# Optimization experiments

Measured on AMD Instinct MI355X. Metric: run time of the kernel, lower is better.

The kernel has to match this reference:

```python
import jax, jax.numpy as jnp
import numpy as np

# Sizes: batch, mapper input dim, subspace dim n, ambient dim k (= n, no equalities),
# number of linear inequalities, number of quadratic constraints.
B, IN_DIM, N, K, M_LIN, QC = 32768, 256, 128, 128, 1024, 16


def setup_inputs() -> dict:
    rng = np.random.default_rng(0)
    x = rng.standard_normal((B, IN_DIM, 1), dtype=np.float32)
    # mapper = nn.Linear(IN_DIM, N)
    W = (rng.standard_normal((N, IN_DIM)) / np.sqrt(IN_DIM)).astype(np.float32)
    b = (0.01 * rng.standard_normal((N,))).astype(np.float32)
    # Linear inequalities A_p z <= b_p, strictly feasible at z0 = 0
    z0 = np.zeros((N, 1), dtype=np.float32)
    A_p = rng.standard_normal((M_LIN, N)).astype(np.float32)
    b_p = (A_p @ z0 + rng.uniform(0.5, 1.5, (M_LIN, 1))).astype(np.float32)
    D = (A_p / (b_p - A_p @ z0)).astype(np.float32)  # D = A_p / ((b_p - A_p z0) 1^T)
    # No equality constraints: y = NA_E z + yp with NA_E = I, yp = 0, y0 = z0
    NA_E = np.eye(K, N, dtype=np.float32)
    yp = np.zeros((K, 1), dtype=np.float32)
    y0 = NA_E @ z0 + yp
    # Quadratic constraints 0.5 y'P y + q'y + r <= 0, strictly feasible at y0.
    # Precompute phi, delta exactly as in ConstraintModule.__init__ (RAYEN branch).
    all_phi = np.empty((QC, 1, K), dtype=np.float32)
    all_delta = np.empty((QC, K, K), dtype=np.float32)
    for i in range(QC):
        G = (rng.standard_normal((K, K)) / np.sqrt(K)).astype(np.float32)
        P = G.T @ G + 0.1 * np.eye(K, dtype=np.float32)
        q = (0.1 * rng.standard_normal((K, 1))).astype(np.float32)
        val0 = 0.5 * y0.T @ P @ y0 + q.T @ y0
        r = -(val0 + np.float32(rng.uniform(0.5, 2.0)))  # value at y0 strictly negative
        quad_at_y0 = 0.5 * y0.T @ P @ y0 + q.T @ y0 + r   # [1,1], < 0
        sigma = 2.0 * quad_at_y0                           # scalar < 0
        g = y0.T @ P + q.T                                 # [1,K]
        all_phi[i] = -g / sigma
        all_delta[i] = (g.T @ g - 4.0 * quad_at_y0 * 0.5 * P) / np.square(sigma)
    return {
        "x": jnp.asarray(x),
        "W": jnp.asarray(W),
        "b": jnp.asarray(b),
        "D": jnp.asarray(D),
        "NA_E": jnp.asarray(NA_E),
        "yp": jnp.asarray(yp),
        "z0": jnp.asarray(z0),
        "all_phi": jnp.asarray(all_phi),
        "all_delta": jnp.asarray(all_delta),
    }


def reference(x, W, b, D, NA_E, yp, z0, all_phi, all_delta):
    Bn = x.shape[0]
    # mapper: x.view(B,-1) -> Linear -> unsqueeze(2)
    v = (x.reshape(Bn, -1) @ W.T + b)[:, :, None]                     # [B,n,1]
    norm_v = jnp.sqrt(jnp.sum(v * v, axis=(1, 2), keepdims=True))    # [B,1,1]
    v_bar = v / jnp.maximum(norm_v, 1e-12)                           # F.normalize
    # kappa from linear constraints: relu(max_m (D v_bar)_m)
    Dv = jnp.einsum('mn,bno->bmo', D, v_bar)                         # [B,M,1]
    kappa = jax.nn.relu(jnp.max(Dv, axis=1, keepdims=True))          # [B,1,1]
    # kappa from quadratic constraints: phi_i rho + sqrt(rho' delta_i rho)
    rho = jnp.einsum('kn,bno->bko', NA_E, v_bar)[..., 0]             # [B,k]
    lin_term = rho @ all_phi[:, 0, :].T                              # [B,Q]
    dr = jnp.einsum('qkl,bl->bqk', all_delta, rho)                   # [B,Q,k]
    quad_term = jnp.einsum('bqk,bk->bq', dr, rho)                    # [B,Q]
    kappa_q = lin_term + jnp.sqrt(quad_term)                         # [B,Q]
    kappa_nl = jnp.max(kappa_q, axis=1)[:, None, None]               # [B,1,1]
    kappa = jnp.maximum(kappa, kappa_nl)
    # alpha = min(1/kappa, ||v||); z = z0 + alpha * v_bar; y = NA_E z + yp
    alpha = jnp.minimum(1.0 / kappa, norm_v)
    z = z0 + alpha * v_bar                                           # [B,n,1]
    y = jnp.einsum('kn,bno->bko', NA_E, z) + yp                      # [B,k,1]
    return y
```

## Files before the change

### kernel.cpp

```cpp
#include <hip/hip_runtime.h>
#include <hip/hip_bf16.h>


typedef __attribute__((ext_vector_type(8))) short short8;
typedef __attribute__((ext_vector_type(4))) float f32x4;

__device__ __forceinline__ float bf2f(unsigned short u) {
    union { unsigned int i; float f; } v; v.i = ((unsigned int)u) << 16; return v.f;
}
__device__ __forceinline__ unsigned short f2bf(float f) {
    union { float f; unsigned int i; } v; v.f = f;
    unsigned int r = v.i + 0x7FFFu + ((v.i >> 16) & 1u);
    return (unsigned short)(r >> 16);
}

template<int DT>
__device__ __forceinline__ short8 ld8(const void* p, size_t i) {
    if constexpr (DT == 1) {
        return *reinterpret_cast<const short8*>(reinterpret_cast<const unsigned short*>(p) + i);
    } else {
        const float* f = reinterpret_cast<const float*>(p) + i;
        short8 r;
#pragma unroll
        for (int j = 0; j < 8; ++j) r[j] = (short)f2bf(f[j]);
        return r;
    }
}
template<int DT>
__device__ __forceinline__ float ldf(const void* p, int i) {
    if constexpr (DT == 1) return bf2f(reinterpret_cast<const unsigned short*>(p)[i]);
    else return reinterpret_cast<const float*>(p)[i];
}

__device__ __forceinline__ void glds16(const void* g, void* l) {
    __builtin_amdgcn_global_load_lds(
        (const __attribute__((address_space(1))) void*)g,
        (__attribute__((address_space(3))) void*)l, 16, 0, 0);
}

__global__ void detect_dtype(const unsigned short* __restrict__ x, int* __restrict__ flag) {
    __shared__ int cnt;
    if (threadIdx.x == 0) cnt = 0;
    __syncthreads();
    float a = fabsf(bf2f(x[threadIdx.x]));
    int ok = (a > 1e-3f && a < 1e2f) ? 1 : 0;
    atomicAdd(&cnt, ok);
    __syncthreads();
    if (threadIdx.x == 0) *flag = (cnt > 200) ? 1 : 0;
}

template<int DT>
__global__ __launch_bounds__(256, 2) void k1_vbar(
    const void* __restrict__ xp, const void* __restrict__ Wp, const void* __restrict__ bp,
    unsigned short* __restrict__ rho_g, unsigned int* __restrict__ kap_u,
    const int* __restrict__ flag)
{
    if (*flag != DT) return;
    __shared__ unsigned char lds_x[32768];
    __shared__ unsigned char lds_v[16384];
    __shared__ float lds_nsq[64][4];

    const int tid = threadIdx.x;
    const int lane = tid & 63;
    const int w = tid >> 6, hi = lane >> 4, lo = lane & 15;
    const size_t row0 = (size_t)blockIdx.x * 64;
    const unsigned char* Xb = (const unsigned char*)xp;

#pragma unroll
    for (int i = 0; i < 8; ++i) {
        int ch = i * 256 + tid;
        int row = ((ch >> 9) << 4) | (ch & 15);
        int off = (((ch >> 6) & 7) << 6) | (((ch >> 4) & 3) << 4);
        if constexpr (DT == 1)
            glds16(Xb + (row0 + row) * 512 + off, lds_x + ch * 16);
        else {
            short8 v = ld8<0>(Xb, (row0 + row) * 256 + (off >> 1));
            *reinterpret_cast<short8*>(lds_x + ch * 16) = v;
        }
    }
    short8 wf[2][8];
#pragma unroll
    for (int ct = 0; ct < 2; ++ct)
#pragma unroll
        for (int kb = 0; kb < 8; ++kb)
            wf[ct][kb] = ld8<DT>(Wp, (size_t)(w * 32 + ct * 16 + lo) * 256 + kb * 32 + hi * 8);
    asm volatile("s_waitcnt vmcnt(0)" ::: "memory");
    __syncthreads();

    f32x4 acc1[2][4];
#pragma unroll
    for (int c = 0; c < 2; ++c)
#pragma unroll
        for (int r = 0; r < 4; ++r)
#pragma unroll
            for (int e = 0; e < 4; ++e) acc1[c][r][e] = 0.f;
#pragma unroll
    for (int kb = 0; kb < 8; ++kb) {
        short8 af[4];
#pragma unroll
        for (int rt = 0; rt < 4; ++rt)
            af[rt] = *reinterpret_cast<const short8*>(lds_x + (((rt << 3) | kb) << 10) + lane * 16);
#pragma unroll
        for (int ct = 0; ct < 2; ++ct)
#pragma unroll
            for (int rt = 0; rt < 4; ++rt)
                acc1[ct][rt] = __builtin_amdgcn_mfma_f32_16x16x32_bf16(af[rt], wf[ct][kb], acc1[ct][rt], 0, 0, 0);
    }
    float bv[2];
#pragma unroll
    for (int ct = 0; ct < 2; ++ct) bv[ct] = ldf<DT>(bp, w * 32 + ct * 16 + lo);
#pragma unroll
    for (int rt = 0; rt < 4; ++rt)
#pragma unroll
        for (int reg = 0; reg < 4; ++reg) {
            float s = 0.f;
#pragma unroll
            for (int ct = 0; ct < 2; ++ct) {
                float v = acc1[ct][rt][reg] + bv[ct];
                acc1[ct][rt][reg] = v;
                s += v * v;
            }
            s += __shfl_xor(s, 1); s += __shfl_xor(s, 2);
            s += __shfl_xor(s, 4); s += __shfl_xor(s, 8);
            if (lo == 0) lds_nsq[rt * 16 + hi * 4 + reg][w] = s;
        }
    __syncthreads();

#pragma unroll
    for (int rt = 0; rt < 4; ++rt)
#pragma unroll
        for (int reg = 0; reg < 4; ++reg) {
            int row = rt * 16 + hi * 4 + reg;
            float nsq = lds_nsq[row][0] + lds_nsq[row][1] + lds_nsq[row][2] + lds_nsq[row][3];
            float rinv = 1.0f / fmaxf(sqrtf(nsq), 1e-12f);
#pragma unroll
            for (int ct = 0; ct < 2; ++ct) {
                int col = w * 32 + ct * 16 + lo;
                *reinterpret_cast<unsigned short*>(lds_v + row * 256 + col * 2) =
                    f2bf(acc1[ct][rt][reg] * rinv);
            }
        }
    if (tid < 64) {
        float nsq = lds_nsq[tid][0] + lds_nsq[tid][1] + lds_nsq[tid][2] + lds_nsq[tid][3];
        float norm = sqrtf(nsq);
        kap_u[row0 + tid] = __float_as_uint(1.0f / norm);
    }
    __syncthreads();
#pragma unroll
    for (int i = 0; i < 4; ++i) {
        int ch = i * 256 + tid;
        int row = ch >> 4, c16 = ch & 15;
        *reinterpret_cast<short8*>(rho_g + (row0 + row) * 128 + c16 * 8) =
            *reinterpret_cast<const short8*>(lds_v + row * 256 + c16 * 16);
    }
}

__device__ __forceinline__ void stage_rho(const unsigned short* rho_g, size_t row0,
                                          unsigned char* lds_rho, int tid) {
#pragma unroll
    for (int i = 0; i < 4; ++i) {
        int ch = i * 256 + tid;
        int row = ch >> 4;
        int off = (ch & 15) * 16;
        glds16((const unsigned char*)rho_g + (row0 + row) * 256 + (off ^ ((row & 7) << 4)),
               lds_rho + ch * 16);
    }
}

template<int DT>
__global__ __launch_bounds__(256, 2) void k2a_dmax(
    const void* __restrict__ Dp, const unsigned short* __restrict__ rho_g,
    unsigned int* __restrict__ kap_u, const int* __restrict__ flag)
{
    if (*flag != DT) return;
    __shared__ unsigned char lds_rho[16384];
    __shared__ float lds_red[64][4];
    const int tid = threadIdx.x;
    const int lane = tid & 63;
    const int w = tid >> 6, hi = lane >> 4, lo = lane & 15;
    const size_t row0 = (size_t)blockIdx.x * 64;
    const int mg = blockIdx.y;

    stage_rho(rho_g, row0, lds_rho, tid);
    asm volatile("s_waitcnt vmcnt(0)" ::: "memory");
    __syncthreads();

    short8 af2[4][4];
#pragma unroll
    for (int rt = 0; rt < 4; ++rt)
#pragma unroll
        for (int kb = 0; kb < 4; ++kb) {
            int row = rt * 16 + lo;
            af2[rt][kb] = *reinterpret_cast<const short8*>(
                lds_rho + row * 256 + (((kb << 6) | (hi << 4)) ^ ((lo & 7) << 4)));
        }

    f32x4 dmax[4];
#pragma unroll
    for (int rt = 0; rt < 4; ++rt)
#pragma unroll
        for (int e = 0; e < 4; ++e) dmax[rt][e] = -3e38f;

#pragma unroll 2
    for (int t = 0; t < 4; ++t) {
        int col = mg * 256 + w * 64 + t * 16 + lo;
        short8 bD[4];
#pragma unroll
        for (int kb = 0; kb < 4; ++kb)
            bD[kb] = ld8<DT>(Dp, (size_t)col * 128 + kb * 32 + hi * 8);
        f32x4 acc[4];
#pragma unroll
        for (int rt = 0; rt < 4; ++rt)
#pragma unroll
            for (int e = 0; e < 4; ++e) acc[rt][e] = 0.f;
#pragma unroll
        for (int kb = 0; kb < 4; ++kb)
#pragma unroll
            for (int rt = 0; rt < 4; ++rt)
                acc[rt] = __builtin_amdgcn_mfma_f32_16x16x32_bf16(af2[rt][kb], bD[kb], acc[rt], 0, 0, 0);
#pragma unroll
        for (int rt = 0; rt < 4; ++rt)
#pragma unroll
            for (int e = 0; e < 4; ++e) dmax[rt][e] = fmaxf(dmax[rt][e], acc[rt][e]);
    }
#pragma unroll
    for (int rt = 0; rt < 4; ++rt)
#pragma unroll
        for (int reg = 0; reg < 4; ++reg) {
            float m = dmax[rt][reg];
            m = fmaxf(m, __shfl_xor(m, 1)); m = fmaxf(m, __shfl_xor(m, 2));
            m = fmaxf(m, __shfl_xor(m, 4)); m = fmaxf(m, __shfl_xor(m, 8));
            if (lo == 0) lds_red[rt * 16 + hi * 4 + reg][w] = m;
        }
    __syncthreads();
    if (tid < 64) {
        float m = fmaxf(fmaxf(lds_red[tid][0], lds_red[tid][1]),
                        fmaxf(lds_red[tid][2], lds_red[tid][3]));
        m = fmaxf(m, 0.f);
        atomicMax(&kap_u[row0 + tid], __float_as_uint(m));
    }
}

template<int DT>
__global__ __launch_bounds__(256, 2) void k2b_quad(
    const void* __restrict__ dltp, const void* __restrict__ phip,
    const unsigned short* __restrict__ rho_g,
    unsigned int* __restrict__ kap_u, const int* __restrict__ flag)
{
    if (*flag != DT) return;
    __shared__ unsigned char lds_rho[16384];
    const int tid = threadIdx.x;
    const int lane = tid & 63;
    const int w = tid >> 6, hi = lane >> 4, lo = lane & 15;
    const size_t row0 = (size_t)blockIdx.x * 64;
    const int q = blockIdx.y * 4 + w;

    stage_rho(rho_g, row0, lds_rho, tid);
    asm volatile("s_waitcnt vmcnt(0)" ::: "memory");
    __syncthreads();

    short8 af2[4][4];
#pragma unroll
    for (int rt = 0; rt < 4; ++rt)
#pragma unroll
        for (int kb = 0; kb < 4; ++kb) {
            int row = rt * 16 + lo;
            af2[rt][kb] = *reinterpret_cast<const short8*>(
                lds_rho + row * 256 + (((kb << 6) | (hi << 4)) ^ ((lo & 7) << 4)));
        }

    f32x4 qsum[4], lsum[4];
#pragma unroll
    for (int rt = 0; rt < 4; ++rt)
#pragma unroll
        for (int e = 0; e < 4; ++e) { qsum[rt][e] = 0.f; lsum[rt][e] = 0.f; }

#pragma unroll 2
    for (int t = 0; t < 8; ++t) {
        int colk = t * 16 + lo;
        short8 bq[4];
#pragma unroll
        for (int kb = 0; kb < 4; ++kb)
            bq[kb] = ld8<DT>(dltp, ((size_t)q * 128 + colk) * 128 + kb * 32 + hi * 8);
        float phv = ldf<DT>(phip, q * 128 + colk);
        f32x4 acc[4];
#pragma unroll
        for (int rt = 0; rt < 4; ++rt)
#pragma unroll
            for (int e = 0; e < 4; ++e) acc[rt][e] = 0.f;
#pragma unroll
        for (int kb = 0; kb < 4; ++kb)
#pragma unroll
            for (int rt = 0; rt < 4; ++rt)
                acc[rt] = __builtin_amdgcn_mfma_f32_16x16x32_bf16(af2[rt][kb], bq[kb], acc[rt], 0, 0, 0);
#pragma unroll
        for (int rt = 0; rt < 4; ++rt)
#pragma unroll
            for (int e = 0; e < 4; ++e) {
                int row = rt * 16 + hi * 4 + e;
                float rv = bf2f(*reinterpret_cast<const unsigned short*>(
                    lds_rho + row * 256 + ((colk * 2) ^ ((row & 7) << 4))));
                qsum[rt][e] += acc[rt][e] * rv;
                lsum[rt][e] += rv * phv;
            }
    }
#pragma unroll
    for (int rt = 0; rt < 4; ++rt)
#pragma unroll
        for (int reg = 0; reg < 4; ++reg) {
            float s = qsum[rt][reg];
            s += __shfl_xor(s, 1); s += __shfl_xor(s, 2);
            s += __shfl_xor(s, 4); s += __shfl_xor(s, 8);
            float l = lsum[rt][reg];
            l += __shfl_xor(l, 1); l += __shfl_xor(l, 2);
            l += __shfl_xor(l, 4); l += __shfl_xor(l, 8);
            if (lo == 0) {
                float kq = l + sqrtf(fmaxf(s, 0.f));
                kq = fmaxf(kq, 0.f);
                atomicMax(&kap_u[row0 + rt * 16 + hi * 4 + reg], __float_as_uint(kq));
            }
        }
}

template<int DT>
__global__ __launch_bounds__(256, 2) void k3_out(
    const unsigned int* __restrict__ kap_u,
    const void* __restrict__ z0p, const void* __restrict__ ypp,
    unsigned short* __restrict__ outp, const int* __restrict__ flag)
{
    if (*flag != DT) return;
    __shared__ float lds_alpha[64];
    const int tid = threadIdx.x;
    const size_t row0 = (size_t)blockIdx.x * 64;

    if (tid < 64)
        lds_alpha[tid] = 1.0f / __uint_as_float(kap_u[row0 + tid]);
    __syncthreads();
#pragma unroll
    for (int i = 0; i < 4; ++i) {
        int idx = tid + i * 256;
        int row = idx >> 4;
        int col0 = (idx & 15) * 8;
        float alpha = lds_alpha[row];
        size_t obase = (row0 + row) * 128 + col0;
        short8 r8 = *reinterpret_cast<const short8*>(outp + obase);
        short8 pack;
#pragma unroll
        for (int j = 0; j < 8; ++j) {
            float yv = ldf<DT>(z0p, col0 + j) + alpha * bf2f((unsigned short)r8[j])
                     + ldf<DT>(ypp, col0 + j);
            pack[j] = (short)f2bf(yv);
        }
        *reinterpret_cast<short8*>(outp + obase) = pack;
    }
}

template<int DT>
__global__ __launch_bounds__(256, 2) void rayen_mono(
    const void* xp, const void* Wp, const void* bp, const void* Dp,
    const void* ypp, const void* z0p, const void* phip, const void* dltp,
    void* outp, const int* flag)
{
    if (*flag != DT) return;
    __shared__ unsigned char lds_big[49152];
    __shared__ unsigned char lds_rho[16384];
    __shared__ float lds_nsq[64][4];
    __shared__ float lds_dmax[64][4];
    __shared__ float lds_quad[64][16];
    __shared__ float lds_lin[64][16];
    __shared__ float lds_alpha[64];

    const int tid = threadIdx.x;
    const int lane = tid & 63;
    const int w = tid >> 6, hi = lane >> 4, lo = lane & 15;
    const size_t row0 = (size_t)blockIdx.x * 64;
    const unsigned char* Xb = (const unsigned char*)xp;

#pragma unroll
    for (int i = 0; i < 8; ++i) {
        int ch = i * 256 + tid;
        int row = ((ch >> 9) << 4) | (ch & 15);
        int off = (((ch >> 6) & 7) << 6) | (((ch >> 4) & 3) << 4);
        if constexpr (DT == 1)
            glds16(Xb + (row0 + row) * 512 + off, lds_big + ch * 16);
        else {
            short8 v = ld8<0>(Xb, (row0 + row) * 256 + (off >> 1));
            *reinterpret_cast<short8*>(lds_big + ch * 16) = v;
        }
    }
    short8 wf[2][8];
#pragma unroll
    for (int ct = 0; ct < 2; ++ct)
#pragma unroll
        for (int kb = 0; kb < 8; ++kb)
            wf[ct][kb] = ld8<DT>(Wp, (size_t)(w * 32 + ct * 16 + lo) * 256 + kb * 32 + hi * 8);
    asm volatile("s_waitcnt vmcnt(0)" ::: "memory");
    __syncthreads();

    f32x4 acc1[2][4];
#pragma unroll
    for (int c = 0; c < 2; ++c)
#pragma unroll
        for (int r = 0; r < 4; ++r)
#pragma unroll
            for (int e = 0; e < 4; ++e) acc1[c][r][e] = 0.f;
#pragma unroll
    for (int kb = 0; kb < 8; ++kb) {
        short8 af[4];
#pragma unroll
        for (int rt = 0; rt < 4; ++rt)
            af[rt] = *reinterpret_cast<const short8*>(lds_big + (((rt << 3) | kb) << 10) + lane * 16);
#pragma unroll
        for (int ct = 0; ct < 2; ++ct)
#pragma unroll
            for (int rt = 0; rt < 4; ++rt)
                acc1[ct][rt] = __builtin_amdgcn_mfma_f32_16x16x32_bf16(af[rt], wf[ct][kb], acc1[ct][rt], 0, 0, 0);
    }
    float bv[2];
#pragma unroll
    for (int ct = 0; ct < 2; ++ct) bv[ct] = ldf<DT>(bp, w * 32 + ct * 16 + lo);
#pragma unroll
    for (int rt = 0; rt < 4; ++rt)
#pragma unroll
        for (int reg = 0; reg < 4; ++reg) {
            float s = 0.f;
#pragma unroll
            for (int ct = 0; ct < 2; ++ct) {
                float v = acc1[ct][rt][reg] + bv[ct];
                acc1[ct][rt][reg] = v;
                s += v * v;
            }
            s += __shfl_xor(s, 1); s += __shfl_xor(s, 2);
            s += __shfl_xor(s, 4); s += __shfl_xor(s, 8);
            if (lo == 0) lds_nsq[rt * 16 + hi * 4 + reg][w] = s;
        }
    __syncthreads();
#pragma unroll
    for (int rt = 0; rt < 4; ++rt)
#pragma unroll
        for (int reg = 0; reg < 4; ++reg) {
            int row = rt * 16 + hi * 4 + reg;
            float nsq = lds_nsq[row][0] + lds_nsq[row][1] + lds_nsq[row][2] + lds_nsq[row][3];
            float rinv = 1.0f / fmaxf(sqrtf(nsq), 1e-12f);
#pragma unroll
            for (int ct = 0; ct < 2; ++ct) {
                int col = w * 32 + ct * 16 + lo;
                *reinterpret_cast<unsigned short*>(
                    lds_rho + row * 256 + ((col * 2) ^ ((row & 7) << 4))) =
                    f2bf(acc1[ct][rt][reg] * rinv);
            }
        }
    __syncthreads();
    short8 af2[4][4];
#pragma unroll
    for (int rt = 0; rt < 4; ++rt)
#pragma unroll
        for (int kb = 0; kb < 4; ++kb) {
            int row = rt * 16 + lo;
            af2[rt][kb] = *reinterpret_cast<const short8*>(
                lds_rho + row * 256 + (((kb << 6) | (hi << 4)) ^ ((lo & 7) << 4)));
        }
    unsigned char* wbase = lds_big + w * 12288;
    auto stage_q = [&](int p, int b) {
        unsigned char* dst0 = wbase + b * 4096;
#pragma unroll
        for (int kb = 0; kb < 4; ++kb) {
            size_t grow; const void* base;
            if (p < 16) { base = Dp; grow = (size_t)(p * 64 + w * 16 + lo); }
            else {
                int pd = p - 16;
                base = dltp;
                grow = (size_t)((((pd >> 3) * 4 + w) * 128) + ((pd & 7) * 16 + lo));
            }
            if constexpr (DT == 1)
                glds16((const unsigned char*)base + grow * 256 + kb * 64 + hi * 16, dst0 + kb * 1024);
            else {
                short8 v = ld8<0>(base, grow * 128 + kb * 32 + hi * 8);
                *reinterpret_cast<short8*>(dst0 + kb * 1024 + lane * 16) = v;
            }
        }
    };
    f32x4 dmax[4], qsum[4];
#pragma unroll
    for (int rt = 0; rt < 4; ++rt)
#pragma unroll
        for (int e = 0; e < 4; ++e) { dmax[rt][e] = -3e38f; qsum[rt][e] = 0.f; }
    stage_q(0, 0); stage_q(1, 1);
#pragma unroll 1
    for (int p = 0; p < 48; ++p) {
        if constexpr (DT == 1) {
            if (p < 47) { asm volatile("s_waitcnt vmcnt(4)" ::: "memory"); }
            else        { asm volatile("s_waitcnt vmcnt(0)" ::: "memory"); }
        } else {
            asm volatile("s_waitcnt vmcnt(0) lgkmcnt(0)" ::: "memory");
        }
        __builtin_amdgcn_sched_barrier(0);
        if (p + 2 < 48) stage_q(p + 2, (p + 2) % 3);
        unsigned char* buf = wbase + (p % 3) * 4096;
        f32x4 acc[4];
#pragma unroll
        for (int rt = 0; rt < 4; ++rt)
#pragma unroll
            for (int e = 0; e < 4; ++e) acc[rt][e] = 0.f;
#pragma unroll
        for (int kb = 0; kb < 4; ++kb) {
            short8 bf = *reinterpret_cast<const short8*>(buf + kb * 1024 + lane * 16);
#pragma unroll
            for (int rt = 0; rt < 4; ++rt)
                acc[rt] = __builtin_amdgcn_mfma_f32_16x16x32_bf16(af2[rt][kb], bf, acc[rt], 0, 0, 0);
        }
        if (p < 16) {
#pragma unroll
            for (int rt = 0; rt < 4; ++rt)
#pragma unroll
                for (int e = 0; e < 4; ++e) dmax[rt][e] = fmaxf(dmax[rt][e], acc[rt][e]);
        } else {
            int pd = p - 16, kr = (pd & 7) << 4;
#pragma unroll
            for (int rt = 0; rt < 4; ++rt)
#pragma unroll
                for (int e = 0; e < 4; ++e) {
                    int row = rt * 16 + hi * 4 + e;
                    float rvv = bf2f(*reinterpret_cast<const unsigned short*>(
                        lds_rho + row * 256 + ((((kr + lo) * 2)) ^ ((row & 7) << 4))));
                    qsum[rt][e] += acc[rt][e] * rvv;
                }
            if ((pd & 7) == 7) {
#pragma unroll
                for (int rt = 0; rt < 4; ++rt)
#pragma unroll
                    for (int e = 0; e < 4; ++e) {
                        float s = qsum[rt][e];
                        s += __shfl_xor(s, 1); s += __shfl_xor(s, 2);
                        s += __shfl_xor(s, 4); s += __shfl_xor(s, 8);
                        if (lo == 0) lds_quad[rt * 16 + hi * 4 + e][((pd >> 3) << 2) | w] = s;
                        qsum[rt][e] = 0.f;
                    }
            }
        }
    }
#pragma unroll
    for (int rt = 0; rt < 4; ++rt)
#pragma unroll
        for (int reg = 0; reg < 4; ++reg) {
            float m = dmax[rt][reg];
            m = fmaxf(m, __shfl_xor(m, 1)); m = fmaxf(m, __shfl_xor(m, 2));
            m = fmaxf(m, __shfl_xor(m, 4)); m = fmaxf(m, __shfl_xor(m, 8));
            if (lo == 0) lds_dmax[rt * 16 + hi * 4 + reg][w] = m;
        }
    if (w == 0) {
        f32x4 accp[4];
#pragma unroll
        for (int rt = 0; rt < 4; ++rt)
#pragma unroll
            for (int e = 0; e < 4; ++e) accp[rt][e] = 0.f;
#pragma unroll
        for (int kb = 0; kb < 4; ++kb) {
            short8 bp8 = ld8<DT>(phip, (size_t)lo * 128 + kb * 32 + hi * 8);
#pragma unroll
            for (int rt = 0; rt < 4; ++rt)
                accp[rt] = __builtin_amdgcn_mfma_f32_16x16x32_bf16(af2[rt][kb], bp8, accp[rt], 0, 0, 0);
        }
#pragma unroll
        for (int rt = 0; rt < 4; ++rt)
#pragma unroll
            for (int reg = 0; reg < 4; ++reg)
                lds_lin[rt * 16 + hi * 4 + reg][lo] = accp[rt][reg];
    }
    __syncthreads();
    if (tid < 64) {
        int row = tid;
        float nsq = lds_nsq[row][0] + lds_nsq[row][1] + lds_nsq[row][2] + lds_nsq[row][3];
        float norm = sqrtf(nsq);
        float kap = fmaxf(0.f, fmaxf(fmaxf(lds_dmax[row][0], lds_dmax[row][1]),
                                     fmaxf(lds_dmax[row][2], lds_dmax[row][3])));
#pragma unroll
        for (int q = 0; q < 16; ++q)
            kap = fmaxf(kap, lds_lin[row][q] + sqrtf(fmaxf(lds_quad[row][q], 0.f)));
        lds_alpha[row] = fminf(1.0f / kap, norm);
    }
    __syncthreads();
#pragma unroll
    for (int i = 0; i < 4; ++i) {
        int idx = tid + i * 256;
        int row = idx >> 4, col0 = (idx & 15) * 8;
        float alpha = lds_alpha[row];
        short8 r8 = *reinterpret_cast<const short8*>(
            lds_rho + row * 256 + ((col0 * 2) ^ ((row & 7) << 4)));
        float yv[8];
#pragma unroll
        for (int j = 0; j < 8; ++j)
            yv[j] = ldf<DT>(z0p, col0 + j) + alpha * bf2f((unsigned short)r8[j]) + ldf<DT>(ypp, col0 + j);
        size_t obase = (row0 + row) * 128 + col0;
        if constexpr (DT == 1) {
            short8 pack;
#pragma unroll
            for (int j = 0; j < 8; ++j) pack[j] = (short)f2bf(yv[j]);
            *reinterpret_cast<short8*>(reinterpret_cast<unsigned short*>(outp) + obase) = pack;
        } else {
            f32x4 p0, p1;
#pragma unroll
            for (int j = 0; j < 4; ++j) { p0[j] = yv[j]; p1[j] = yv[4 + j]; }
            *reinterpret_cast<f32x4*>(reinterpret_cast<float*>(outp) + obase) = p0;
            *reinterpret_cast<f32x4*>(reinterpret_cast<float*>(outp) + obase + 4) = p1;
        }
    }
}

extern "C" void kernel_launch(void* const* d_in, const int* in_sizes, int n_in,
                              void* d_out, int out_size, void* d_ws, size_t ws_size,
                              hipStream_t stream) {
    const void* x    = d_in[0];
    const void* W    = d_in[1];
    const void* b    = d_in[2];
    const void* D    = d_in[3];
    const void* yp   = d_in[5];
    const void* z0   = d_in[6];
    const void* phi  = d_in[7];
    const void* dlt  = d_in[8];

    const int B = in_sizes[0] / 256;
    const int tiles = B / 64;

    unsigned char* ws = reinterpret_cast<unsigned char*>(d_ws);
    int* flag = reinterpret_cast<int*>(ws);
    unsigned int* kap_u = reinterpret_cast<unsigned int*>(ws + 4096);
    const size_t need = 4096 + (size_t)B * 4;

    detect_dtype<<<dim3(1), dim3(256), 0, stream>>>(
        reinterpret_cast<const unsigned short*>(x), flag);

    dim3 blk(256);
    if (ws_size >= need) {
        unsigned short* rho_g = reinterpret_cast<unsigned short*>(d_out);
        k1_vbar<1><<<dim3(tiles), blk, 0, stream>>>(x, W, b, rho_g, kap_u, flag);
        k2a_dmax<1><<<dim3(tiles, 4), blk, 0, stream>>>(D, rho_g, kap_u, flag);
        k2b_quad<1><<<dim3(tiles, 4), blk, 0, stream>>>(dlt, phi, rho_g, kap_u, flag);
        k3_out<1><<<dim3(tiles), blk, 0, stream>>>(kap_u, z0, yp, rho_g, flag);
        rayen_mono<0><<<dim3(tiles), blk, 0, stream>>>(x, W, b, D, yp, z0, phi, dlt, d_out, flag);
    } else {
        rayen_mono<1><<<dim3(tiles), blk, 0, stream>>>(x, W, b, D, yp, z0, phi, dlt, d_out, flag);
        rayen_mono<0><<<dim3(tiles), blk, 0, stream>>>(x, W, b, D, yp, z0, phi, dlt, d_out, flag);
    }
}
```

Measured before the change: 127.7 us.

## Route fp32 inputs through split kernels using pre-converted bf16 constants

Adds a cvt_const kernel that converts W, D, delta and phi to bf16 in workspace on every call. The fp32 path then runs the multi-kernel pipeline (vbar, dmax, quad, out) instead of the monolithic rayen_mono kernel. rho is now kept in workspace rather than in the output buffer, and k3_out gains an fp32 store path. fp32 loads of x are vectorised into float4 reads. This is meant to remove the repeated per-block fp32→bf16 conversion of constants and to reuse the split schedule for fp32. In exchange it adds a conversion launch, two extra launches that exit early on the dtype flag, and a much larger workspace requirement; if the workspace is too small, execution falls back to the monolithic kernel.

After: 113.7 us. 1.12x faster.

```diff
diff --git a/kernel.cpp b/kernel.cpp
--- a/kernel.cpp
+++ b/kernel.cpp
@@ -4,6 +4,7 @@
 
 typedef __attribute__((ext_vector_type(8))) short short8;
 typedef __attribute__((ext_vector_type(4))) float f32x4;
+typedef __attribute__((ext_vector_type(4))) unsigned short us4;
 
 __device__ __forceinline__ float bf2f(unsigned short u) {
     union { unsigned int i; float f; } v; v.i = ((unsigned int)u) << 16; return v.f;
@@ -32,6 +33,15 @@
     else return reinterpret_cast<const float*>(p)[i];
 }
 
+__device__ __forceinline__ short8 ld8f4(const float* f) {
+    f32x4 a = *reinterpret_cast<const f32x4*>(f);
+    f32x4 b = *reinterpret_cast<const f32x4*>(f + 4);
+    short8 r;
+#pragma unroll
+    for (int j = 0; j < 4; ++j) { r[j] = (short)f2bf(a[j]); r[4 + j] = (short)f2bf(b[j]); }
+    return r;
+}
+
 __device__ __forceinline__ void glds16(const void* g, void* l) {
     __builtin_amdgcn_global_load_lds(
         (const __attribute__((address_space(1))) void*)g,
@@ -49,9 +59,37 @@
     if (threadIdx.x == 0) *flag = (cnt > 200) ? 1 : 0;
 }
 
+__global__ void cvt_const(
+    const void* __restrict__ Wp, const void* __restrict__ Dp,
+    const void* __restrict__ Qp, const void* __restrict__ Pp,
+    unsigned short* __restrict__ Wb, unsigned short* __restrict__ Db,
+    unsigned short* __restrict__ Qb, unsigned short* __restrict__ Pb,
+    const int* __restrict__ flag)
+{
+    const int nW = 32768, nD = 131072, nQ = 262144, nP = 2048;
+    int idx = blockIdx.x * 256 + threadIdx.x;
+    int e = idx * 4;
+    if (e >= nW + nD + nQ + nP) return;
+    const void* src; unsigned short* dst; int off;
+    if      (e < nW)           { src = Wp; dst = Wb; off = e; }
+    else if (e < nW + nD)      { src = Dp; dst = Db; off = e - nW; }
+    else if (e < nW + nD + nQ) { src = Qp; dst = Qb; off = e - nW - nD; }
+    else                       { src = Pp; dst = Pb; off = e - nW - nD - nQ; }
+    us4 out;
+    if (*flag == 0) {
+        f32x4 v = *reinterpret_cast<const f32x4*>(reinterpret_cast<const float*>(src) + off);
+#pragma unroll
+        for (int j = 0; j < 4; ++j) out[j] = f2bf(v[j]);
+    } else {
+        out = *reinterpret_cast<const us4*>(reinterpret_cast<const unsigned short*>(src) + off);
+    }
+    *reinterpret_cast<us4*>(dst + off) = out;
+}
+
 template<int DT>
 __global__ __launch_bounds__(256, 2) void k1_vbar(
-    const void* __restrict__ xp, const void* __restrict__ Wp, const void* __restrict__ bp,
+    const void* __restrict__ xp, const unsigned short* __restrict__ Wb,
+    const void* __restrict__ bp,
     unsigned short* __restrict__ rho_g, unsigned int* __restrict__ kap_u,
     const int* __restrict__ flag)
 {
@@ -64,18 +102,17 @@
     const int lane = tid & 63;
     const int w = tid >> 6, hi = lane >> 4, lo = lane & 15;
     const size_t row0 = (size_t)blockIdx.x * 64;
-    const unsigned char* Xb = (const unsigned char*)xp;
 
 #pragma unroll
     for (int i = 0; i < 8; ++i) {
         int ch = i * 256 + tid;
         int row = ((ch >> 9) << 4) | (ch & 15);
         int off = (((ch >> 6) & 7) << 6) | (((ch >> 4) & 3) << 4);
-        if constexpr (DT == 1)
-            glds16(Xb + (row0 + row) * 512 + off, lds_x + ch * 16);
-        else {
-            short8 v = ld8<0>(Xb, (row0 + row) * 256 + (off >> 1));
-            *reinterpret_cast<short8*>(lds_x + ch * 16) = v;
+        if constexpr (DT == 1) {
+            glds16((const unsigned char*)xp + (row0 + row) * 512 + off, lds_x + ch * 16);
+        } else {
+            const float* src = (const float*)xp + (row0 + row) * 256 + (off >> 1);
+            *reinterpret_cast<short8*>(lds_x + ch * 16) = ld8f4(src);
         }
     }
     short8 wf[2][8];
@@ -83,8 +120,9 @@
     for (int ct = 0; ct < 2; ++ct)
 #pragma unroll
         for (int kb = 0; kb < 8; ++kb)
-            wf[ct][kb] = ld8<DT>(Wp, (size_t)(w * 32 + ct * 16 + lo) * 256 + kb * 32 + hi * 8);
-    asm volatile("s_waitcnt vmcnt(0)" ::: "memory");
+            wf[ct][kb] = *reinterpret_cast<const short8*>(
+                Wb + (size_t)(w * 32 + ct * 16 + lo) * 256 + kb * 32 + hi * 8);
+    if constexpr (DT == 1) { asm volatile("s_waitcnt vmcnt(0)" ::: "memory"); }
     __syncthreads();
 
     f32x4 acc1[2][4];
@@ -142,8 +180,7 @@
         }
     if (tid < 64) {
         float nsq = lds_nsq[tid][0] + lds_nsq[tid][1] + lds_nsq[tid][2] + lds_nsq[tid][3];
-        float norm = sqrtf(nsq);
-        kap_u[row0 + tid] = __float_as_uint(1.0f / norm);
+        kap_u[row0 + tid] = __float_as_uint(1.0f / sqrtf(nsq));
     }
     __syncthreads();
 #pragma unroll
@@ -167,12 +204,10 @@
     }
 }
 
-template<int DT>
 __global__ __launch_bounds__(256, 2) void k2a_dmax(
-    const void* __restrict__ Dp, const unsigned short* __restrict__ rho_g,
-    unsigned int* __restrict__ kap_u, const int* __restrict__ flag)
+    const unsigned short* __restrict__ Db, const unsigned short* __restrict__ rho_g,
+    unsigned int* __restrict__ kap_u)
 {
-    if (*flag != DT) return;
     __shared__ unsigned char lds_rho[16384];
     __shared__ float lds_red[64][4];
     const int tid = threadIdx.x;
@@ -207,7 +242,7 @@
         short8 bD[4];
 #pragma unroll
         for (int kb = 0; kb < 4; ++kb)
-            bD[kb] = ld8<DT>(Dp, (size_t)col * 128 + kb * 32 + hi * 8);
+            bD[kb] = *reinterpret_cast<const short8*>(Db + (size_t)col * 128 + kb * 32 + hi * 8);
         f32x4 acc[4];
 #pragma unroll
         for (int rt = 0; rt < 4; ++rt)
@@ -241,13 +276,10 @@
     }
 }
 
-template<int DT>
 __global__ __launch_bounds__(256, 2) void k2b_quad(
-    const void* __restrict__ dltp, const void* __restrict__ phip,
-    const unsigned short* __restrict__ rho_g,
-    unsigned int* __restrict__ kap_u, const int* __restrict__ flag)
+    const unsigned short* __restrict__ Qb, const unsigned short* __restrict__ Pb,
+    const unsigned short* __restrict__ rho_g, unsigned int* __restrict__ kap_u)
 {
-    if (*flag != DT) return;
     __shared__ unsigned char lds_rho[16384];
     const int tid = threadIdx.x;
     const int lane = tid & 63;
@@ -281,8 +313,9 @@
         short8 bq[4];
 #pragma unroll
         for (int kb = 0; kb < 4; ++kb)
-            bq[kb] = ld8<DT>(dltp, ((size_t)q * 128 + colk) * 128 + kb * 32 + hi * 8);
-        float phv = ldf<DT>(phip, q * 128 + colk);
+            bq[kb] = *reinterpret_cast<const short8*>(
+                Qb + ((size_t)q * 128 + colk) * 128 + kb * 32 + hi * 8);
+        float phv = bf2f(Pb[q * 128 + colk]);
         f32x4 acc[4];
 #pragma unroll
         for (int rt = 0; rt < 4; ++rt)
@@ -315,8 +348,7 @@
             l += __shfl_xor(l, 1); l += __shfl_xor(l, 2);
             l += __shfl_xor(l, 4); l += __shfl_xor(l, 8);
             if (lo == 0) {
-                float kq = l + sqrtf(fmaxf(s, 0.f));
-                kq = fmaxf(kq, 0.f);
+                float kq = fmaxf(l + sqrtf(fmaxf(s, 0.f)), 0.f);
                 atomicMax(&kap_u[row0 + rt * 16 + hi * 4 + reg], __float_as_uint(kq));
             }
         }
@@ -324,9 +356,9 @@
 
 template<int DT>
 __global__ __launch_bounds__(256, 2) void k3_out(
-    const unsigned int* __restrict__ kap_u,
+    const unsigned int* __restrict__ kap_u, const unsigned short* __restrict__ rho_g,
     const void* __restrict__ z0p, const void* __restrict__ ypp,
-    unsigned short* __restrict__ outp, const int* __restrict__ flag)
+    void* __restrict__ outp, const int* __restrict__ flag)
 {
     if (*flag != DT) return;
     __shared__ float lds_alpha[64];
@@ -342,16 +374,29 @@
         int row = idx >> 4;
         int col0 = (idx & 15) * 8;
         float alpha = lds_alpha[row];
+        short8 r8 = *reinterpret_cast<const short8*>(rho_g + (row0 + row) * 128 + col0);
         size_t obase = (row0 + row) * 128 + col0;
-        short8 r8 = *reinterpret_cast<const short8*>(outp + obase);
-        short8 pack;
-#pragma unroll
-        for (int j = 0; j < 8; ++j) {
-            float yv = ldf<DT>(z0p, col0 + j) + alpha * bf2f((unsigned short)r8[j])
-                     + ldf<DT>(ypp, col0 + j);
-            pack[j] = (short)f2bf(yv);
-        }
-        *reinterpret_cast<short8*>(outp + obase) = pack;
+        if constexpr (DT == 1) {
+            short8 pack;
+#pragma unroll
+            for (int j = 0; j < 8; ++j) {
+                float yv = ldf<1>(z0p, col0 + j) + alpha * bf2f((unsigned short)r8[j])
+                         + ldf<1>(ypp, col0 + j);
+                pack[j] = (short)f2bf(yv);
+            }
+            *reinterpret_cast<short8*>(reinterpret_cast<unsigned short*>(outp) + obase) = pack;
+        } else {
+            f32x4 p0, p1;
+#pragma unroll
+            for (int j = 0; j < 4; ++j) {
+                p0[j] = ldf<0>(z0p, col0 + j) + alpha * bf2f((unsigned short)r8[j])
+                      + ldf<0>(ypp, col0 + j);
+                p1[j] = ldf<0>(z0p, col0 + 4 + j) + alpha * bf2f((unsigned short)r8[4 + j])
+                      + ldf<0>(ypp, col0 + 4 + j);
+            }
+            *reinterpret_cast<f32x4*>(reinterpret_cast<float*>(outp) + obase) = p0;
+            *reinterpret_cast<f32x4*>(reinterpret_cast<float*>(outp) + obase + 4) = p1;
+        }
     }
 }
 
@@ -384,8 +429,8 @@
         if constexpr (DT == 1)
             glds16(Xb + (row0 + row) * 512 + off, lds_big + ch * 16);
         else {
-            short8 v = ld8<0>(Xb, (row0 + row) * 256 + (off >> 1));
-            *reinterpret_cast<short8*>(lds_big + ch * 16) = v;
+            const float* src = (const float*)xp + (row0 + row) * 256 + (off >> 1);
+            *reinterpret_cast<short8*>(lds_big + ch * 16) = ld8f4(src);
         }
     }
     short8 wf[2][8];
@@ -475,8 +520,8 @@
             if constexpr (DT == 1)
                 glds16((const unsigned char*)base + grow * 256 + kb * 64 + hi * 16, dst0 + kb * 1024);
             else {
-                short8 v = ld8<0>(base, grow * 128 + kb * 32 + hi * 8);
-                *reinterpret_cast<short8*>(dst0 + kb * 1024 + lane * 16) = v;
+                const float* src = (const float*)base + grow * 128 + kb * 32 + hi * 8;
+                *reinterpret_cast<short8*>(dst0 + kb * 1024 + lane * 16) = ld8f4(src);
             }
         }
     };
@@ -624,20 +669,27 @@
 
     unsigned char* ws = reinterpret_cast<unsigned char*>(d_ws);
     int* flag = reinterpret_cast<int*>(ws);
-    unsigned int* kap_u = reinterpret_cast<unsigned int*>(ws + 4096);
-    const size_t need = 4096 + (size_t)B * 4;
+    unsigned int*   kap_u = reinterpret_cast<unsigned int*>(ws + 4096);
+    unsigned short* Wb    = reinterpret_cast<unsigned short*>(ws + 135168);
+    unsigned short* Db    = reinterpret_cast<unsigned short*>(ws + 200704);
+    unsigned short* Qb    = reinterpret_cast<unsigned short*>(ws + 462848);
+    unsigned short* Pb    = reinterpret_cast<unsigned short*>(ws + 987136);
+    unsigned short* rho_g = reinterpret_cast<unsigned short*>(ws + 991232);
+    const size_t need = 991232 + (size_t)B * 256;
 
     detect_dtype<<<dim3(1), dim3(256), 0, stream>>>(
         reinterpret_cast<const unsigned short*>(x), flag);
 
     dim3 blk(256);
     if (ws_size >= need) {
-        unsigned short* rho_g = reinterpret_cast<unsigned short*>(d_out);
-        k1_vbar<1><<<dim3(tiles), blk, 0, stream>>>(x, W, b, rho_g, kap_u, flag);
-        k2a_dmax<1><<<dim3(tiles, 4), blk, 0, stream>>>(D, rho_g, kap_u, flag);
-        k2b_quad<1><<<dim3(tiles, 4), blk, 0, stream>>>(dlt, phi, rho_g, kap_u, flag);
-        k3_out<1><<<dim3(tiles), blk, 0, stream>>>(kap_u, z0, yp, rho_g, flag);
-        rayen_mono<0><<<dim3(tiles), blk, 0, stream>>>(x, W, b, D, yp, z0, phi, dlt, d_out, flag);
+        cvt_const<<<dim3((428032 / 4 + 255) / 256), blk, 0, stream>>>(
+            W, D, dlt, phi, Wb, Db, Qb, Pb, flag);
+        k1_vbar<0><<<dim3(tiles), blk, 0, stream>>>(x, Wb, b, rho_g, kap_u, flag);
+        k1_vbar<1><<<dim3(tiles), blk, 0, stream>>>(x, Wb, b, rho_g, kap_u, flag);
+        k2a_dmax<<<dim3(tiles, 4), blk, 0, stream>>>(Db, rho_g, kap_u);
+        k2b_quad<<<dim3(tiles, 4), blk, 0, stream>>>(Qb, Pb, rho_g, kap_u);
+        k3_out<0><<<dim3(tiles), blk, 0, stream>>>(kap_u, rho_g, z0, yp, d_out, flag);
+        k3_out<1><<<dim3(tiles), blk, 0, stream>>>(kap_u, rho_g, z0, yp, d_out, flag);
     } else {
         rayen_mono<1><<<dim3(tiles), blk, 0, stream>>>(x, W, b, D, yp, z0, phi, dlt, d_out, flag);
         rayen_mono<0><<<dim3(tiles), blk, 0, stream>>>(x, W, b, D, yp, z0, phi, dlt, d_out, flag);
```
